# Kernel tuning notes

Measured on AMD Instinct MI355X. Metric: run time of the kernel, lower is better.

Reference implementation:

```python
import jax, jax.numpy as jnp
import numpy as np

B, C, H, W = 4, 384, 56, 56
K, S = 5, 7


def setup_inputs() -> dict:
    key = jax.random.key(0)
    k1, k2, k3, k4, k5 = jax.random.split(key, 5)
    x = jax.random.normal(k1, (B, C, H, W), dtype=jnp.float32)
    ctx = jax.random.normal(k2, (B, C, H, W), dtype=jnp.float32)
    # 1x1 conv weights stored as (out_ch, in_ch) matrices
    Wq = jax.random.normal(k3, (C // 2, C), dtype=jnp.float32) * (1.0 / np.sqrt(C))
    Wk = jax.random.normal(k4, (C // 2, C), dtype=jnp.float32) * (1.0 / np.sqrt(C))
    Wwd = jax.random.normal(k5, (K * K, S * S), dtype=jnp.float32) * (1.0 / np.sqrt(S * S))
    return {"x": x, "ctx": ctx, "Wq": Wq, "Wk": Wk, "Wwd": Wwd}


def reference(x, ctx, Wq, Wk, Wwd):
    b, c, h, w = x.shape
    kk = K
    # q: 1x1 conv then flatten spatial -> (B, C/2, HW)
    q = jnp.einsum('dc,bchw->bdhw', Wq, x).reshape(b, c // 2, h * w)
    # adaptive avg pool to S x S (H,W multiples of S -> uniform 8x8 bins)
    ctx_p = ctx.reshape(b, c, S, h // S, S, w // S).mean(axis=(3, 5))  # (B,C,S,S)
    kf = jnp.einsum('dc,bcst->bdst', Wk, ctx_p).reshape(b, c // 2, S * S)
    # attention over region centers: (B, HW, S*S)
    A = jax.nn.softmax(jnp.einsum('bdn,bds->bns', q, kf), axis=-1)
    # dynamic per-pixel kernels via 1x1 conv S*S -> k*k: (B, k*k, H, W)
    dyn = jnp.einsum('js,bns->bjn', Wwd, A).reshape(b, kk * kk, h, w)
    # unfold x (im2col with padding k//2) -> (B, C, k*k, H, W)
    pad = kk // 2
    xp = jnp.pad(x, ((0, 0), (0, 0), (pad, pad), (pad, pad)))
    patches = jnp.stack(
        [xp[:, :, i:i + h, j:j + w] for i in range(kk) for j in range(kk)], axis=2
    )
    # per-pixel weighted reduction over the k*k taps
    out = jnp.einsum('bcjhw,bjhw->bchw', patches, dyn)
    return out
```

## Files before the change

### kernel.cpp

```cpp
#include <hip/hip_runtime.h>

#define BB 4
#define CCH 384
#define HH 56
#define WWD 56
#define HW 3136
#define S2 49
#define S2P 52
#define D2 192
#define K2 25
#define XSP 20

__global__ __launch_bounds__(256) void gt_k(const float* __restrict__ Wk,
                                            const float* __restrict__ Wq,
                                            float* __restrict__ GT) {
    __shared__ float As[D2 * 16];
    __shared__ float Bs[D2 * 16];
    int bi = blockIdx.x % 24, bj = blockIdx.x / 24;
    int t = threadIdx.x;
    int tj = t & 15, ti = t >> 4;
#pragma unroll
    for (int k = 0; k < 3; k++) {
        int idx = t + 256 * k;
        int d = idx >> 2, q = idx & 3;
        *(float4*)&As[idx * 4] = *(const float4*)&Wk[(size_t)d * CCH + bi * 16 + 4 * q];
        *(float4*)&Bs[idx * 4] = *(const float4*)&Wq[(size_t)d * CCH + bj * 16 + 4 * q];
    }
    __syncthreads();
    float acc = 0.f;
#pragma unroll 8
    for (int d = 0; d < D2; d++)
        acc += As[d * 16 + ti] * Bs[d * 16 + tj];
    GT[(size_t)(bi * 16 + ti) * CCH + bj * 16 + tj] = acc;
}

__global__ __launch_bounds__(384) void mv_k(const float* __restrict__ ctx,
                                            const float* __restrict__ GT,
                                            float* __restrict__ M) {
    __shared__ float v[CCH];
    int b = blockIdx.x / S2, s = blockIdx.x % S2;
    int t = threadIdx.x;
    int sy = s / 7, sx = s % 7;
    {
        const float* p = ctx + ((size_t)(b * CCH + t)) * HW + sy * 8 * WWD + sx * 8;
        float sum = 0.f;
#pragma unroll
        for (int r = 0; r < 8; r++) {
            float4 a = *(const float4*)(p + r * WWD);
            float4 c = *(const float4*)(p + r * WWD + 4);
            sum += a.x + a.y + a.z + a.w + c.x + c.y + c.z + c.w;
        }
        v[t] = sum * (1.f / 64.f);
    }
    __syncthreads();
    float acc = 0.f;
#pragma unroll 8
    for (int i = 0; i < CCH; i++)
        acc += v[i] * GT[(size_t)i * CCH + t];
    M[((size_t)(b * CCH + t)) * S2P + s] = acc;
    if (s < 3) M[((size_t)(b * CCH + t)) * S2P + 49 + s] = 0.f;
}

__global__ __launch_bounds__(256) void attn_k(const float* __restrict__ x,
                                              const float* __restrict__ M,
                                              const float* __restrict__ Wwd,
                                              float* __restrict__ dyn) {
    __shared__ __align__(16) float smem[96 * XSP + 96 * S2P];
    __shared__ __align__(16) float sc[16 * S2P];
    __shared__ __align__(16) float wl[K2 * S2P];
    float* xs  = smem;
    float* Ms  = smem + 96 * XSP;
    float* red = smem;

    int b  = blockIdx.x / 196;
    int n0 = (blockIdx.x % 196) * 16;
    int t  = threadIdx.x;
    int pxg = t & 3, sg = (t >> 2) & 3, slice = t >> 4;

    float4 acc4[4][4];
#pragma unroll
    for (int k = 0; k < 4; k++)
#pragma unroll
        for (int j = 0; j < 4; j++) acc4[k][j] = make_float4(0.f, 0.f, 0.f, 0.f);

    const float* xb = x + (size_t)b * CCH * HW + n0;
    const float* Mb = M + (size_t)b * CCH * S2P;

    for (int ch = 0; ch < 4; ch++) {
        int c0 = ch * 96;
        {
            int idx = t;
            int r = idx >> 2, cq = idx & 3;
            float4 val = *(const float4*)&xb[(size_t)(c0 + r) * HW + 4 * cq];
            *(float4*)&xs[r * XSP + 4 * cq] = val;
            if (t < 128) {
                int idx2 = t + 256;
                int r2 = idx2 >> 2, cq2 = idx2 & 3;
                float4 v2 = *(const float4*)&xb[(size_t)(c0 + r2) * HW + 4 * cq2];
                *(float4*)&xs[r2 * XSP + 4 * cq2] = v2;
            }
        }
        {
            const float* src = Mb + (size_t)c0 * S2P;
#pragma unroll
            for (int k = 0; k < 4; k++) {
                int idx = t + 256 * k;
                *(float4*)&Ms[4 * idx] = *(const float4*)&src[4 * idx];
            }
            if (t < 224) {
                int idx = t + 1024;
                *(float4*)&Ms[4 * idx] = *(const float4*)&src[4 * idx];
            }
        }
        __syncthreads();
        int rbase = 6 * slice;
#pragma unroll
        for (int m = 0; m < 6; m++) {
            int r = rbase + m;
            const float4 xv = *(const float4*)&xs[r * XSP + 4 * pxg];
#pragma unroll
            for (int k = 0; k < 3; k++) {
                int g = sg + 4 * k;
                const float4 mv = *(const float4*)&Ms[r * S2P + 4 * g];
                acc4[k][0].x += mv.x * xv.x; acc4[k][0].y += mv.x * xv.y;
                acc4[k][0].z += mv.x * xv.z; acc4[k][0].w += mv.x * xv.w;
                acc4[k][1].x += mv.y * xv.x; acc4[k][1].y += mv.y * xv.y;
                acc4[k][1].z += mv.y * xv.z; acc4[k][1].w += mv.y * xv.w;
                acc4[k][2].x += mv.z * xv.x; acc4[k][2].y += mv.z * xv.y;
                acc4[k][2].z += mv.z * xv.z; acc4[k][2].w += mv.z * xv.w;
                acc4[k][3].x += mv.w * xv.x; acc4[k][3].y += mv.w * xv.y;
                acc4[k][3].z += mv.w * xv.z; acc4[k][3].w += mv.w * xv.w;
            }
            if (sg == 0) {
                const float4 mv = *(const float4*)&Ms[r * S2P + 48];
                acc4[3][0].x += mv.x * xv.x; acc4[3][0].y += mv.x * xv.y;
                acc4[3][0].z += mv.x * xv.z; acc4[3][0].w += mv.x * xv.w;
                acc4[3][1].x += mv.y * xv.x; acc4[3][1].y += mv.y * xv.y;
                acc4[3][1].z += mv.y * xv.z; acc4[3][1].w += mv.y * xv.w;
                acc4[3][2].x += mv.z * xv.x; acc4[3][2].y += mv.z * xv.y;
                acc4[3][2].z += mv.z * xv.z; acc4[3][2].w += mv.z * xv.w;
                acc4[3][3].x += mv.w * xv.x; acc4[3][3].y += mv.w * xv.y;
                acc4[3][3].z += mv.w * xv.z; acc4[3][3].w += mv.w * xv.w;
            }
        }
        __syncthreads();
    }

#pragma unroll
    for (int k = 0; k < 4; k++)
#pragma unroll
        for (int j = 0; j < 4; j++) {
            acc4[k][j].x += __shfl_xor(acc4[k][j].x, 16);
            acc4[k][j].y += __shfl_xor(acc4[k][j].y, 16);
            acc4[k][j].z += __shfl_xor(acc4[k][j].z, 16);
            acc4[k][j].w += __shfl_xor(acc4[k][j].w, 16);
            acc4[k][j].x += __shfl_xor(acc4[k][j].x, 32);
            acc4[k][j].y += __shfl_xor(acc4[k][j].y, 32);
            acc4[k][j].z += __shfl_xor(acc4[k][j].z, 32);
            acc4[k][j].w += __shfl_xor(acc4[k][j].w, 32);
        }

    if ((t & 63) < 16) {
        int wv = t >> 6;
        float* rb = red + (size_t)wv * 16 * S2P;
#pragma unroll
        for (int k = 0; k < 4; k++) {
            int g = sg + 4 * k;
            if (g < 13) {
                *(float4*)&rb[(4 * pxg + 0) * S2P + 4 * g] =
                    make_float4(acc4[k][0].x, acc4[k][1].x, acc4[k][2].x, acc4[k][3].x);
                *(float4*)&rb[(4 * pxg + 1) * S2P + 4 * g] =
                    make_float4(acc4[k][0].y, acc4[k][1].y, acc4[k][2].y, acc4[k][3].y);
                *(float4*)&rb[(4 * pxg + 2) * S2P + 4 * g] =
                    make_float4(acc4[k][0].z, acc4[k][1].z, acc4[k][2].z, acc4[k][3].z);
                *(float4*)&rb[(4 * pxg + 3) * S2P + 4 * g] =
                    make_float4(acc4[k][0].w, acc4[k][1].w, acc4[k][2].w, acc4[k][3].w);
            }
        }
    }
    __syncthreads();

    if (t < 208) {
        int px = t / 13, q = t - px * 13;
        float4 ssum = make_float4(0.f, 0.f, 0.f, 0.f);
#pragma unroll
        for (int wv = 0; wv < 4; wv++) {
            float4 vv = *(float4*)&red[(size_t)(wv * 16 + px) * S2P + 4 * q];
            ssum.x += vv.x; ssum.y += vv.y; ssum.z += vv.z; ssum.w += vv.w;
        }
        *(float4*)&sc[px * S2P + 4 * q] = ssum;
    }
    __syncthreads();

    if (t < 128) {
        int px = t >> 3, li = t & 7;
        float mx = -3.4e38f;
#pragma unroll
        for (int k = 0; k < 7; k++) { int s = li + 8 * k; if (s < S2) mx = fmaxf(mx, sc[px * S2P + s]); }
        mx = fmaxf(mx, __shfl_xor(mx, 1, 8));
        mx = fmaxf(mx, __shfl_xor(mx, 2, 8));
        mx = fmaxf(mx, __shfl_xor(mx, 4, 8));
        float e[7]; float sum = 0.f;
#pragma unroll
        for (int k = 0; k < 7; k++) {
            int s = li + 8 * k;
            if (s < S2) { e[k] = __expf(sc[px * S2P + s] - mx); sum += e[k]; }
        }
        sum += __shfl_xor(sum, 1, 8);
        sum += __shfl_xor(sum, 2, 8);
        sum += __shfl_xor(sum, 4, 8);
        float inv = 1.f / sum;
#pragma unroll
        for (int k = 0; k < 7; k++) {
            int s = li + 8 * k;
            if (s < S2) sc[px * S2P + s] = e[k] * inv;
        }
    } else {
        int u = t - 128;
#pragma unroll
        for (int k = 0; k < 10; k++) {
            int i = u + 128 * k;
            int j = i / S2P, ss = i - j * S2P;
            wl[i] = (ss < S2) ? Wwd[j * S2 + ss] : 0.f;
        }
        if (u < 20) {
            int i = u + 1280;
            int j = i / S2P, ss = i - j * S2P;
            wl[i] = (ss < S2) ? Wwd[j * S2 + ss] : 0.f;
        }
    }
    __syncthreads();

    float* dynb = dyn + (size_t)b * K2 * HW + n0;
#pragma unroll
    for (int pass = 0; pass < 2; pass++) {
        int o = t + 256 * pass;
        if (pass == 0 || t < 144) {
            int j = o >> 4, px = o & 15;
            float a = 0.f;
#pragma unroll
            for (int q = 0; q < 13; q++) {
                float4 wv = *(float4*)&wl[j * S2P + 4 * q];
                float4 pv = *(float4*)&sc[px * S2P + 4 * q];
                a += wv.x * pv.x + wv.y * pv.y + wv.z * pv.z + wv.w * pv.w;
            }
            dynb[(size_t)j * HW + px] = a;
        }
    }
}

__global__ __launch_bounds__(256, 3) void out_k(const float* __restrict__ x,
                                                const float* __restrict__ dyn,
                                                float* __restrict__ out) {
    __shared__ float xt[16][12][60];
    int blk    = blockIdx.x;
    int stripe = blk % 7;
    int cg     = (blk / 7) % 24;
    int b      = blk / (7 * 24);
    int h0 = stripe * 8;
    int c0 = cg * 16;
    int t  = threadIdx.x;
    const float* xb = x + ((size_t)(b * CCH + c0)) * HW;

    if (t < 192) {
        int cc = t / 12, r = t % 12;
        xt[cc][r][0] = 0.f; xt[cc][r][1] = 0.f;
        xt[cc][r][58] = 0.f; xt[cc][r][59] = 0.f;
    }
#pragma unroll
    for (int k = 0; k < 11; k++) {
        int idx = t + 256 * k;
        if (k < 10 || t < 128) {
            int cc  = idx / 168;
            int rem = idx - cc * 168;
            int r   = rem / 14;
            int q   = rem - r * 14;
            int h   = h0 - 2 + r;
            float4 v = make_float4(0.f, 0.f, 0.f, 0.f);
            if ((unsigned)h < (unsigned)HH)
                v = *(const float4*)&xb[(size_t)cc * HW + h * WWD + 4 * q];
            xt[cc][r][2 + 4 * q + 0] = v.x;
            xt[cc][r][2 + 4 * q + 1] = v.y;
            xt[cc][r][2 + 4 * q + 2] = v.z;
            xt[cc][r][2 + 4 * q + 3] = v.w;
        }
    }

    bool act = t < 224;
    int w = t % 56;
    int u = t / 56;
    int n = (h0 + 2 * u) * WWD + w;
    float dv0[K2], dv1[K2];
    if (act) {
        const float* db = dyn + (size_t)b * K2 * HW + n;
#pragma unroll
        for (int j = 0; j < K2; j++) {
            dv0[j] = db[(size_t)j * HW];
            dv1[j] = db[(size_t)j * HW + WWD];
        }
    }
    __syncthreads();
    if (!act) return;

    float* ob = out + ((size_t)(b * CCH + c0)) * HW + n;
#pragma unroll
    for (int cc = 0; cc < 16; cc++) {
        float a0 = 0.f, a1 = 0.f;
#pragma unroll
        for (int rr = 0; rr < 6; rr++) {
            int lr = 2 * u + rr;
            float v0 = xt[cc][lr][w + 0];
            float v1 = xt[cc][lr][w + 1];
            float v2 = xt[cc][lr][w + 2];
            float v3 = xt[cc][lr][w + 3];
            float v4 = xt[cc][lr][w + 4];
            if (rr < 5) {
                int o5 = rr * 5;
                a0 += v0 * dv0[o5] + v1 * dv0[o5 + 1] + v2 * dv0[o5 + 2]
                    + v3 * dv0[o5 + 3] + v4 * dv0[o5 + 4];
            }
            if (rr >= 1) {
                int o5 = (rr - 1) * 5;
                a1 += v0 * dv1[o5] + v1 * dv1[o5 + 1] + v2 * dv1[o5 + 2]
                    + v3 * dv1[o5 + 3] + v4 * dv1[o5 + 4];
            }
        }
        ob[(size_t)cc * HW] = a0;
        ob[(size_t)cc * HW + WWD] = a1;
    }
}

extern "C" void kernel_launch(void* const* d_in, const int* in_sizes, int n_in,
                              void* d_out, int out_size, void* d_ws, size_t ws_size,
                              hipStream_t stream) {
    const float* x   = (const float*)d_in[0];
    const float* ctx = (const float*)d_in[1];
    const float* Wq  = (const float*)d_in[2];
    const float* Wk  = (const float*)d_in[3];
    const float* Wwd = (const float*)d_in[4];
    float* out = (float*)d_out;
    float* ws  = (float*)d_ws;

    float* GT  = ws;
    float* M   = ws + 147456;
    float* dyn = ws + 147456 + 79872;

    gt_k<<<24 * 24, 256, 0, stream>>>(Wk, Wq, GT);
    mv_k<<<BB * S2, 384, 0, stream>>>(ctx, GT, M);
    attn_k<<<BB * 196, 256, 0, stream>>>(x, M, Wwd, dyn);
    out_k<<<BB * 24 * 7, 256, 0, stream>>>(x, dyn, out);
}
```

Measured before the change: 161.6 us.

## Software-pipeline global loads through registers in mv_k and attn_k

mv_k now stages the GT matrix through shared memory in 64-row chunks, prefetching the next chunk into registers while computing on the current one, and uses four partial accumulators. attn_k double-buffers its x and M tile loads in registers so the next channel chunk's global loads overlap the current FMA work. The Wwd table load is hoisted to the kernel start and spread over all threads. The aim is to hide global memory latency, at the cost of more registers and an extra 96KB of shared memory in mv_k, which may reduce occupancy.

```diff
diff --git a/kernel.cpp b/kernel.cpp
--- a/kernel.cpp
+++ b/kernel.cpp
@@ -10,6 +10,7 @@
 #define D2 192
 #define K2 25
 #define XSP 20
+#define MVCH 64
 
 __global__ __launch_bounds__(256) void gt_k(const float* __restrict__ Wk,
                                             const float* __restrict__ Wq,
@@ -38,8 +39,16 @@
                                             const float* __restrict__ GT,
                                             float* __restrict__ M) {
     __shared__ float v[CCH];
+    __shared__ float gs[MVCH * CCH];
     int b = blockIdx.x / S2, s = blockIdx.x % S2;
     int t = threadIdx.x;
+    float4 pr[16];
+#pragma unroll
+    for (int k = 0; k < 16; k++) {
+        int idx4 = t + 384 * k;
+        int r = idx4 / 96, cq = idx4 - r * 96;
+        pr[k] = *(const float4*)&GT[(size_t)r * CCH + 4 * cq];
+    }
     int sy = s / 7, sx = s % 7;
     {
         const float* p = ctx + ((size_t)(b * CCH + t)) * HW + sy * 8 * WWD + sx * 8;
@@ -52,11 +61,41 @@
         }
         v[t] = sum * (1.f / 64.f);
     }
-    __syncthreads();
-    float acc = 0.f;
-#pragma unroll 8
-    for (int i = 0; i < CCH; i++)
-        acc += v[i] * GT[(size_t)i * CCH + t];
+#pragma unroll
+    for (int k = 0; k < 16; k++) {
+        int idx4 = t + 384 * k;
+        *(float4*)&gs[4 * idx4] = pr[k];
+    }
+    __syncthreads();
+    float a0 = 0.f, a1 = 0.f, a2 = 0.f, a3 = 0.f;
+    for (int c = 0; c < 6; c++) {
+        if (c < 5) {
+#pragma unroll
+            for (int k = 0; k < 16; k++) {
+                int idx4 = t + 384 * k;
+                int r = idx4 / 96, cq = idx4 - r * 96;
+                pr[k] = *(const float4*)&GT[(size_t)((c + 1) * MVCH + r) * CCH + 4 * cq];
+            }
+        }
+        int i0 = c * MVCH;
+#pragma unroll
+        for (int r = 0; r < MVCH; r += 4) {
+            a0 += v[i0 + r + 0] * gs[(r + 0) * CCH + t];
+            a1 += v[i0 + r + 1] * gs[(r + 1) * CCH + t];
+            a2 += v[i0 + r + 2] * gs[(r + 2) * CCH + t];
+            a3 += v[i0 + r + 3] * gs[(r + 3) * CCH + t];
+        }
+        __syncthreads();
+        if (c < 5) {
+#pragma unroll
+            for (int k = 0; k < 16; k++) {
+                int idx4 = t + 384 * k;
+                *(float4*)&gs[4 * idx4] = pr[k];
+            }
+            __syncthreads();
+        }
+    }
+    float acc = (a0 + a1) + (a2 + a3);
     M[((size_t)(b * CCH + t)) * S2P + s] = acc;
     if (s < 3) M[((size_t)(b * CCH + t)) * S2P + 49 + s] = 0.f;
 }
@@ -86,33 +125,51 @@
     const float* xb = x + (size_t)b * CCH * HW + n0;
     const float* Mb = M + (size_t)b * CCH * S2P;
 
+#pragma unroll
+    for (int k = 0; k < 5; k++) {
+        int i = t + 256 * k;
+        int j = i / S2P, ss = i - j * S2P;
+        wl[i] = (ss < S2) ? Wwd[j * S2 + ss] : 0.f;
+    }
+    if (t < 20) {
+        int i = t + 1280;
+        int j = i / S2P, ss = i - j * S2P;
+        wl[i] = (ss < S2) ? Wwd[j * S2 + ss] : 0.f;
+    }
+
+    int r0 = t >> 2, cq = t & 3;
+    int r1 = (t + 256) >> 2;
+    float4 px0, px1, pm0, pm1, pm2, pm3, pm4;
+
+#define ATTN_LOAD(c0)                                                          \
+    {                                                                          \
+        px0 = *(const float4*)&xb[(size_t)((c0) + r0) * HW + 4 * cq];          \
+        if (t < 128)                                                           \
+            px1 = *(const float4*)&xb[(size_t)((c0) + r1) * HW + 4 * cq];      \
+        const float* srcm = Mb + (size_t)(c0) * S2P;                           \
+        pm0 = *(const float4*)&srcm[4 * t];                                    \
+        pm1 = *(const float4*)&srcm[4 * (t + 256)];                            \
+        pm2 = *(const float4*)&srcm[4 * (t + 512)];                            \
+        pm3 = *(const float4*)&srcm[4 * (t + 768)];                            \
+        if (t < 224) pm4 = *(const float4*)&srcm[4 * (t + 1024)];              \
+    }
+
+#define ATTN_WRITE()                                                           \
+    {                                                                          \
+        *(float4*)&xs[r0 * XSP + 4 * cq] = px0;                                \
+        if (t < 128) *(float4*)&xs[r1 * XSP + 4 * cq] = px1;                   \
+        *(float4*)&Ms[4 * t] = pm0;                                            \
+        *(float4*)&Ms[4 * (t + 256)] = pm1;                                    \
+        *(float4*)&Ms[4 * (t + 512)] = pm2;                                    \
+        *(float4*)&Ms[4 * (t + 768)] = pm3;                                    \
+        if (t < 224) *(float4*)&Ms[4 * (t + 1024)] = pm4;                      \
+    }
+
+    ATTN_LOAD(0);
     for (int ch = 0; ch < 4; ch++) {
-        int c0 = ch * 96;
-        {
-            int idx = t;
-            int r = idx >> 2, cq = idx & 3;
-            float4 val = *(const float4*)&xb[(size_t)(c0 + r) * HW + 4 * cq];
-            *(float4*)&xs[r * XSP + 4 * cq] = val;
-            if (t < 128) {
-                int idx2 = t + 256;
-                int r2 = idx2 >> 2, cq2 = idx2 & 3;
-                float4 v2 = *(const float4*)&xb[(size_t)(c0 + r2) * HW + 4 * cq2];
-                *(float4*)&xs[r2 * XSP + 4 * cq2] = v2;
-            }
-        }
-        {
-            const float* src = Mb + (size_t)c0 * S2P;
-#pragma unroll
-            for (int k = 0; k < 4; k++) {
-                int idx = t + 256 * k;
-                *(float4*)&Ms[4 * idx] = *(const float4*)&src[4 * idx];
-            }
-            if (t < 224) {
-                int idx = t + 1024;
-                *(float4*)&Ms[4 * idx] = *(const float4*)&src[4 * idx];
-            }
-        }
+        ATTN_WRITE();
         __syncthreads();
+        if (ch < 3) { ATTN_LOAD((ch + 1) * 96); }
         int rbase = 6 * slice;
 #pragma unroll
         for (int m = 0; m < 6; m++) {
@@ -215,19 +272,6 @@
             int s = li + 8 * k;
             if (s < S2) sc[px * S2P + s] = e[k] * inv;
         }
-    } else {
-        int u = t - 128;
-#pragma unroll
-        for (int k = 0; k < 10; k++) {
-            int i = u + 128 * k;
-            int j = i / S2P, ss = i - j * S2P;
-            wl[i] = (ss < S2) ? Wwd[j * S2 + ss] : 0.f;
-        }
-        if (u < 20) {
-            int i = u + 1280;
-            int j = i / S2P, ss = i - j * S2P;
-            wl[i] = (ss < S2) ? Wwd[j * S2 + ss] : 0.f;
-        }
     }
     __syncthreads();
 
@@ -247,6 +291,8 @@
             dynb[(size_t)j * HW + px] = a;
         }
     }
+#undef ATTN_LOAD
+#undef ATTN_WRITE
 }
 
 __global__ __launch_bounds__(256, 3) void out_k(const float* __restrict__ x,
```

New measurement: 195.7 us. 1.21x slower.
